# Performance work log

Measured on AMD Instinct MI355X. Metric: run time of the kernel, lower is better.

## Reference

```python
import jax, jax.numpy as jnp
import numpy as np

WS = 8        # window_size
HEADS = 6     # num_heads
DIM = 96      # dim


def _relative_position_index(ws):
    # Static int index table, identical to the torch buffer construction.
    coords = np.stack(np.meshgrid(np.arange(ws), np.arange(ws), indexing='ij'))  # (2, ws, ws)
    cf = coords.reshape(2, -1)                              # (2, N)
    rel = cf[:, :, None] - cf[:, None, :]                   # (2, N, N)
    rel = rel.transpose(1, 2, 0).copy()                     # (N, N, 2)
    rel[:, :, 0] += ws - 1
    rel[:, :, 1] += ws - 1
    rel[:, :, 0] *= 2 * ws - 1
    return rel.sum(-1)                                      # (N, N)


def setup_inputs() -> dict:
    key = jax.random.key(0)
    ks = jax.random.split(key, 6)
    B, C, H, W = 1, DIM, 512, 512
    return {
        'x': jax.random.normal(ks[0], (B, C, H, W), jnp.float32),
        'qkv_w': jax.random.normal(ks[1], (3 * C, C), jnp.float32) * 0.02,
        'qkv_b': jnp.zeros((3 * C,), jnp.float32),
        'dw_w': jax.random.normal(ks[2], (3 * C, 1, 3, 3), jnp.float32) * 0.02,
        'dw_b': jnp.zeros((3 * C,), jnp.float32),
        'proj_w': jax.random.normal(ks[3], (C, C), jnp.float32) * 0.02,
        'proj_b': jnp.zeros((C,), jnp.float32),
        'temperature': jnp.ones((HEADS, 1, 1), jnp.float32),
        'rel_bias_table': jax.random.normal(ks[4], ((2 * WS - 1) ** 2, HEADS), jnp.float32) * 0.02,
    }


def reference(x, qkv_w, qkv_b, dw_w, dw_b, proj_w, proj_b, temperature, rel_bias_table):
    B, C, H, W = x.shape
    ws, heads = WS, HEADS
    N = ws * ws
    hd = C // heads
    scale = hd ** (-0.5)

    # ---- window partition: (B,C,H,W) -> (B*nW, C, ws, ws) ----
    xw = x.reshape(B, C, H // ws, ws, W // ws, ws)
    xw = xw.transpose(0, 2, 4, 1, 3, 5).reshape(-1, C, ws, ws)

    # ---- qkv 1x1 conv + depthwise 3x3 conv ----
    qkv = jnp.einsum('oi,bihw->bohw', qkv_w, xw) + qkv_b[None, :, None, None]
    qkv = jax.lax.conv_general_dilated(
        qkv, dw_w, window_strides=(1, 1), padding='SAME',
        feature_group_count=3 * C,
        dimension_numbers=('NCHW', 'OIHW', 'NCHW')) + dw_b[None, :, None, None]
    q, k, v = jnp.split(qkv, 3, axis=1)

    # (b, head, c, N)
    def to_heads(t):
        return t.reshape(t.shape[0], heads, hd, N)

    q = to_heads(q * scale)
    k = to_heads(k)
    v = to_heads(v)

    # F.normalize(dim=-1): L2 over the spatial (N) axis, eps=1e-12
    q = q / jnp.clip(jnp.linalg.norm(q, axis=-1, keepdims=True), 1e-12)
    k = k / jnp.clip(jnp.linalg.norm(k, axis=-1, keepdims=True), 1e-12)

    # channel attention: (b,h,c,c)
    attn_ch = jnp.einsum('bhcn,bhdn->bhcd', q, k) * temperature
    # spatial attention: (b,h,N,N)
    attn_sp = jnp.einsum('bhcn,bhcm->bhnm', q, k)

    idx = _relative_position_index(ws).reshape(-1)           # (N*N,)
    bias = rel_bias_table[idx].reshape(N, N, heads).transpose(2, 0, 1)  # (h,N,N)
    attn_sp = attn_sp + bias[None]

    attn_ch = jax.nn.softmax(attn_ch, axis=-1)
    attn_sp = jax.nn.softmax(attn_sp, axis=-1)

    # out = attn_channel @ v @ attn : (b,h,c,N)
    out = jnp.einsum('bhcd,bhdn->bhcn', attn_ch, v)
    out = jnp.einsum('bhcn,bhnm->bhcm', out, attn_sp)

    # back to (B*nW, C, ws, ws) then window reverse -> (B,C,H,W)
    out = out.reshape(-1, C, ws, ws)
    out = out.reshape(B, H // ws, W // ws, C, ws, ws)
    out = out.transpose(0, 3, 1, 4, 2, 5).reshape(B, C, H, W)

    # proj 1x1 conv
    out = jnp.einsum('oi,bihw->bohw', proj_w, out) + proj_b[None, :, None, None]
    return out
```

## Files before the change

kernel.cpp:

```cpp
#include <hip/hip_runtime.h>

typedef short short8 __attribute__((ext_vector_type(8)));
typedef float float4v __attribute__((ext_vector_type(4)));

__device__ __forceinline__ unsigned short f2bf(float f) {
    unsigned int u = __float_as_uint(f);
    u += 0x7fffu + ((u >> 16) & 1u);
    return (unsigned short)(u >> 16);
}
__device__ __forceinline__ float bfs(const unsigned short* p) {
    return __uint_as_float(((unsigned int)*p) << 16);
}
__device__ __forceinline__ float4v mfma16(short8 a, short8 b, float4v c) {
    return __builtin_amdgcn_mfma_f32_16x16x32_bf16(a, b, c, 0, 0, 0);
}

__global__ void prep_pack(const float* __restrict__ qkv_w,
                          const float* __restrict__ proj_w,
                          short* __restrict__ apq, short* __restrict__ app) {
    const int i = blockIdx.x * 256 + threadIdx.x;
    if (i < 3456) {
        const int rem = i % 192, f = rem / 64, lane = rem % 64;
        const int m = (i / 192) * 16 + (lane & 15);
        const int kb = f * 32 + ((lane >> 4) & 3) * 8;
        const float* s = qkv_w + m * 96 + kb;
        short8 o;
        #pragma unroll
        for (int j = 0; j < 8; ++j) o[j] = (short)f2bf(s[j]);
        *(short8*)(apq + i * 8) = o;
    } else if (i < 4608) {
        const int i2 = i - 3456;
        const int rem = i2 % 192, f = rem / 64, lane = rem % 64;
        const int m = (i2 / 192) * 16 + (lane & 15);
        const int kb = f * 32 + ((lane >> 4) & 3) * 8;
        const float* s = proj_w + m * 96 + kb;
        short8 o;
        #pragma unroll
        for (int j = 0; j < 8; ++j) o[j] = (short)f2bf(s[j]);
        *(short8*)(app + i2 * 8) = o;
    }
}

__global__ __launch_bounds__(256, 2)
void fused_win_attn(const float* __restrict__ x,
                    const short* __restrict__ apq,
                    const float* __restrict__ qkv_b,
                    const float* __restrict__ dw_w,
                    const float* __restrict__ dw_b,
                    const short* __restrict__ app,
                    const float* __restrict__ proj_b,
                    const float* __restrict__ temperature,
                    const float* __restrict__ rel_bias,
                    float* __restrict__ yout)
{
    __shared__ __align__(16) unsigned char smem[60688];
    unsigned short* sxT   = (unsigned short*)smem;
    unsigned short* soutT = (unsigned short*)(smem + 13312);
    unsigned short* sbias = (unsigned short*)(smem + 26624);
    unsigned short* sqkv  = (unsigned short*)(smem + 29328);
    unsigned short* raw   = (unsigned short*)(smem + 36240);
    unsigned short* sST   = (unsigned short*)(smem + 36240);
    unsigned short* qnT   = (unsigned short*)(smem + 45456);
    unsigned short* knT   = (unsigned short*)(smem + 48528);
    unsigned short* vT    = (unsigned short*)(smem + 51600);
    unsigned short* stmp  = (unsigned short*)(smem + 54672);
    unsigned short* ach   = (unsigned short*)(smem + 56976);
    float*          sdw   = (float*)(smem + 57744);
    float*          sred  = (float*)(smem + 59664);

    const int tid  = threadIdx.x;
    const int lane = tid & 63;
    const int g    = tid >> 6;
    const int quad = lane >> 4;
    const int l15  = lane & 15;
    const int wi   = blockIdx.x;
    const int y0   = (wi >> 6) << 3;
    const int x0   = (wi & 63) << 3;
    const int py   = lane >> 3, px = lane & 7;

    for (int r = tid; r < 1536; r += 256) {
        const int c = r >> 4, q4 = r & 15, p0 = q4 * 4;
        float4 v = *(const float4*)(x + c * 262144 + (y0 + (p0 >> 3)) * 512 + x0 + (p0 & 7));
        sxT[(p0 + 0) * 104 + c] = f2bf(v.x);
        sxT[(p0 + 1) * 104 + c] = f2bf(v.y);
        sxT[(p0 + 2) * 104 + c] = f2bf(v.z);
        sxT[(p0 + 3) * 104 + c] = f2bf(v.w);
    }
    for (int r = tid; r < 1350; r += 256) sbias[r] = f2bf(rel_bias[r]);
    __syncthreads();

    for (int h = 0; h < 6; ++h) {
        for (int r = tid; r < 480; r += 256) {
            const int j = r / 10, t = r % 10;
            const int O = (j >> 4) * 96 + h * 16 + (j & 15);
            sdw[r] = (t < 9) ? dw_w[O * 9 + t] : dw_b[O];
        }
        {
            short8 bf[3];
            #pragma unroll
            for (int f = 0; f < 3; ++f)
                bf[f] = *(const short8*)(sxT + (g * 16 + l15) * 104 + f * 32 + quad * 8);
            #pragma unroll
            for (int t = 0; t < 3; ++t) {
                float4v acc = {0.f, 0.f, 0.f, 0.f};
                #pragma unroll
                for (int f = 0; f < 3; ++f) {
                    short8 af = *(const short8*)(apq + (((t * 6 + h) * 3 + f) * 64 + lane) * 8);
                    acc = mfma16(af, bf[f], acc);
                }
                #pragma unroll
                for (int reg = 0; reg < 4; ++reg) {
                    const int rr = quad * 4 + reg;
                    raw[(t * 16 + rr) * 65 + g * 16 + l15] =
                        f2bf(acc[reg] + qkv_b[t * 96 + h * 16 + rr]);
                }
            }
        }
        __syncthreads();

        #pragma unroll
        for (int r = 0; r < 12; ++r) {
            const int j = g + 4 * r;
            const float v = bfs(raw + j * 65 + lane);
            const float* w = sdw + j * 10;
            float a = w[9];
            #pragma unroll
            for (int di = 0; di < 3; ++di) {
                #pragma unroll
                for (int dj = 0; dj < 3; ++dj) {
                    const int off = (di - 1) * 8 + (dj - 1);
                    const float nb = (off == 0) ? v : __shfl(v, lane + off, 64);
                    const bool ok = ((unsigned)(py + di - 1) < 8u) & ((unsigned)(px + dj - 1) < 8u);
                    a = fmaf(w[di * 3 + dj], ok ? nb : 0.f, a);
                }
            }
            if (j < 32) {
                float ss = a * a;
                #pragma unroll
                for (int m = 1; m < 64; m <<= 1) ss += __shfl_xor(ss, m, 64);
                const float nv = a * (1.f / fmaxf(sqrtf(ss), 1e-12f));
                const unsigned short b = f2bf(nv);
                sqkv[j * 72 + lane] = b;
                if (j < 16) qnT[lane * 24 + j] = b;
                else        knT[lane * 24 + (j - 16)] = b;
            } else {
                vT[lane * 24 + (j - 32)] = f2bf(a);
            }
        }
        __syncthreads();

        float ex[16];
        {
            short8 ak = {0,0,0,0,0,0,0,0};
            if (lane < 32) ak = *(const short8*)(knT + (g * 16 + l15) * 24 + quad * 8);
            #pragma unroll
            for (int nt = 0; nt < 4; ++nt) {
                short8 bq = {0,0,0,0,0,0,0,0};
                if (lane < 32) bq = *(const short8*)(qnT + (nt * 16 + l15) * 24 + quad * 8);
                float4v cs = {0.f, 0.f, 0.f, 0.f};
                cs = mfma16(ak, bq, cs);
                float ps = 0.f;
                #pragma unroll
                for (int reg = 0; reg < 4; ++reg) {
                    const int m = g * 16 + quad * 4 + reg;
                    const int n = nt * 16 + l15;
                    const int idx = ((n >> 3) - (m >> 3) + 7) * 15 + ((n & 7) - (m & 7) + 7);
                    const float e = __expf(cs[reg] + bfs(sbias + idx * 6 + h));
                    ex[nt * 4 + reg] = e;
                    ps += e;
                }
                ps += __shfl_xor(ps, 16, 64);
                ps += __shfl_xor(ps, 32, 64);
                if (lane < 16) sred[g * 64 + nt * 16 + lane] = ps;
            }
        }
        if (g == 0) {
            short8 a0 = *(const short8*)(sqkv + l15 * 72 + quad * 8);
            short8 a1 = *(const short8*)(sqkv + l15 * 72 + 32 + quad * 8);
            short8 b0 = *(const short8*)(sqkv + (16 + l15) * 72 + quad * 8);
            short8 b1 = *(const short8*)(sqkv + (16 + l15) * 72 + 32 + quad * 8);
            float4v cc = {0.f, 0.f, 0.f, 0.f};
            cc = mfma16(a0, b0, cc);
            cc = mfma16(a1, b1, cc);
            const float tp = temperature[h];
            #pragma unroll
            for (int reg = 0; reg < 4; ++reg) {
                const float e = __expf(cc[reg] * tp);
                float se = e;
                #pragma unroll
                for (int m = 1; m < 16; m <<= 1) se += __shfl_xor(se, m, 64);
                ach[(quad * 4 + reg) * 24 + l15] = f2bf(e / se);
            }
        }
        __syncthreads();

        #pragma unroll
        for (int nt = 0; nt < 4; ++nt) {
            const int n = nt * 16 + l15;
            const float inv = 1.f / (sred[n] + sred[64 + n] + sred[128 + n] + sred[192 + n]);
            #pragma unroll
            for (int reg = 0; reg < 4; ++reg)
                sST[(g * 16 + quad * 4 + reg) * 72 + n] = f2bf(ex[nt * 4 + reg] * inv);
        }
        {
            short8 af = {0,0,0,0,0,0,0,0}, bf = {0,0,0,0,0,0,0,0};
            if (lane < 32) {
                af = *(const short8*)(ach + l15 * 24 + quad * 8);
                bf = *(const short8*)(vT + (g * 16 + l15) * 24 + quad * 8);
            }
            float4v ct = {0.f, 0.f, 0.f, 0.f};
            ct = mfma16(af, bf, ct);
            #pragma unroll
            for (int reg = 0; reg < 4; ++reg)
                stmp[(quad * 4 + reg) * 72 + g * 16 + l15] = f2bf(ct[reg]);
        }
        __syncthreads();

        {
            short8 a0 = *(const short8*)(stmp + l15 * 72 + quad * 8);
            short8 a1 = *(const short8*)(stmp + l15 * 72 + 32 + quad * 8);
            short8 b0 = *(const short8*)(sST + (g * 16 + l15) * 72 + quad * 8);
            short8 b1 = *(const short8*)(sST + (g * 16 + l15) * 72 + 32 + quad * 8);
            float4v co = {0.f, 0.f, 0.f, 0.f};
            co = mfma16(a0, b0, co);
            co = mfma16(a1, b1, co);
            #pragma unroll
            for (int reg = 0; reg < 4; ++reg)
                soutT[(g * 16 + l15) * 104 + h * 16 + quad * 4 + reg] = f2bf(co[reg]);
        }
        __syncthreads();
    }

    {
        short8 pb[3];
        #pragma unroll
        for (int f = 0; f < 3; ++f)
            pb[f] = *(const short8*)(soutT + (g * 16 + l15) * 104 + f * 32 + quad * 8);
        const int p = g * 16 + l15;
        float* outbase = yout + (y0 + (p >> 3)) * 512 + x0 + (p & 7);
        #pragma unroll
        for (int mt = 0; mt < 6; ++mt) {
            float4v acc = {0.f, 0.f, 0.f, 0.f};
            #pragma unroll
            for (int f = 0; f < 3; ++f) {
                short8 af = *(const short8*)(app + ((mt * 3 + f) * 64 + lane) * 8);
                acc = mfma16(af, pb[f], acc);
            }
            #pragma unroll
            for (int reg = 0; reg < 4; ++reg) {
                const int o = mt * 16 + quad * 4 + reg;
                outbase[o * 262144] = acc[reg] + proj_b[o];
            }
        }
    }
}

extern "C" void kernel_launch(void* const* d_in, const int* in_sizes, int n_in,
                              void* d_out, int out_size, void* d_ws, size_t ws_size,
                              hipStream_t stream) {
    const float* x      = (const float*)d_in[0];
    const float* qkv_w  = (const float*)d_in[1];
    const float* qkv_b  = (const float*)d_in[2];
    const float* dw_w   = (const float*)d_in[3];
    const float* dw_b   = (const float*)d_in[4];
    const float* proj_w = (const float*)d_in[5];
    const float* proj_b = (const float*)d_in[6];
    const float* temp   = (const float*)d_in[7];
    const float* relb   = (const float*)d_in[8];
    float* o = (float*)d_out;

    short* apq = (short*)d_ws;
    short* app = apq + 27648;

    hipLaunchKernelGGL(prep_pack, dim3(18), dim3(256), 0, stream, qkv_w, proj_w, apq, app);
    hipLaunchKernelGGL(fused_win_attn, dim3(4096), dim3(256), 0, stream,
                       x, apq, qkv_b, dw_w, dw_b, app, proj_b, temp, relb, o);
}
```

Measured before the change: 654.8 us.

## Shrink LDS footprint, pad depthwise conv buffer, and raise occupancy to four blocks

Reorganizes shared memory so buffers alias each other, cutting LDS use from about 60KB to 40KB. This lets launch bounds ask for four resident blocks per CU instead of two. The depthwise 3x3 conv now reads from a zero-padded 10x10 LDS tile with precomputed offsets rather than cross-lane shuffles with boundary masks. Depthwise weights are loaded as wave-uniform scalars from global memory instead of being staged in LDS, and q/k/v are written as packed 4-element stores. Block indices are swizzled to change window traversal order, and the x fragments are hoisted out of the head loop into registers. The tighter register budget at four blocks per CU may cause spills, and the aliased buffers need careful synchronization.

```diff
diff --git a/kernel.cpp b/kernel.cpp
--- a/kernel.cpp
+++ b/kernel.cpp
@@ -41,7 +41,7 @@
     }
 }
 
-__global__ __launch_bounds__(256, 2)
+__global__ __launch_bounds__(256, 4)
 void fused_win_attn(const float* __restrict__ x,
                     const short* __restrict__ apq,
                     const float* __restrict__ qkv_b,
@@ -53,33 +53,33 @@
                     const float* __restrict__ rel_bias,
                     float* __restrict__ yout)
 {
-    __shared__ __align__(16) unsigned char smem[60688];
+    __shared__ __align__(16) unsigned char smem[40080];
     unsigned short* sxT   = (unsigned short*)smem;
+    unsigned short* raw   = (unsigned short*)smem;
+    unsigned short* sST   = (unsigned short*)smem;
+    unsigned short* stmp  = (unsigned short*)(smem + 9216);
+    unsigned short* ach   = (unsigned short*)(smem + 11520);
+    float*          sred  = (float*)(smem + 12288);
     unsigned short* soutT = (unsigned short*)(smem + 13312);
-    unsigned short* sbias = (unsigned short*)(smem + 26624);
-    unsigned short* sqkv  = (unsigned short*)(smem + 29328);
-    unsigned short* raw   = (unsigned short*)(smem + 36240);
-    unsigned short* sST   = (unsigned short*)(smem + 36240);
-    unsigned short* qnT   = (unsigned short*)(smem + 45456);
-    unsigned short* knT   = (unsigned short*)(smem + 48528);
-    unsigned short* vT    = (unsigned short*)(smem + 51600);
-    unsigned short* stmp  = (unsigned short*)(smem + 54672);
-    unsigned short* ach   = (unsigned short*)(smem + 56976);
-    float*          sdw   = (float*)(smem + 57744);
-    float*          sred  = (float*)(smem + 59664);
+    unsigned short* sqkv  = (unsigned short*)(smem + 26624);
+    unsigned short* qnT   = (unsigned short*)(smem + 31232);
+    unsigned short* knT   = (unsigned short*)(smem + 33280);
+    unsigned short* vT    = (unsigned short*)(smem + 35328);
+    unsigned short* sbias = (unsigned short*)(smem + 37376);
 
     const int tid  = threadIdx.x;
     const int lane = tid & 63;
     const int g    = tid >> 6;
     const int quad = lane >> 4;
     const int l15  = lane & 15;
-    const int wi   = blockIdx.x;
-    const int y0   = (wi >> 6) << 3;
-    const int x0   = (wi & 63) << 3;
-    const int py   = lane >> 3, px = lane & 7;
+    const int bx = blockIdx.x;
+    const int wi = (bx & ~15) | ((bx & 7) << 1) | ((bx >> 3) & 1);
+    const int y0 = (wi >> 6) << 3;
+    const int x0 = (wi & 63) << 3;
+    const int py = lane >> 3, px = lane & 7;
 
     for (int r = tid; r < 1536; r += 256) {
-        const int c = r >> 4, q4 = r & 15, p0 = q4 * 4;
+        const int c = r >> 4, p0 = (r & 15) * 4;
         float4 v = *(const float4*)(x + c * 262144 + (y0 + (p0 >> 3)) * 512 + x0 + (p0 & 7));
         sxT[(p0 + 0) * 104 + c] = f2bf(v.x);
         sxT[(p0 + 1) * 104 + c] = f2bf(v.y);
@@ -89,74 +89,93 @@
     for (int r = tid; r < 1350; r += 256) sbias[r] = f2bf(rel_bias[r]);
     __syncthreads();
 
+    short8 bfx[3];
+    #pragma unroll
+    for (int f = 0; f < 3; ++f)
+        bfx[f] = *(const short8*)(sxT + (g * 16 + l15) * 104 + f * 32 + quad * 8);
+    int doff[9];
+    #pragma unroll
+    for (int di = 0; di < 3; ++di)
+        #pragma unroll
+        for (int dj = 0; dj < 3; ++dj)
+            doff[di * 3 + dj] = (py + di) * 10 + (px + dj);
+    __syncthreads();
+
     for (int h = 0; h < 6; ++h) {
-        for (int r = tid; r < 480; r += 256) {
-            const int j = r / 10, t = r % 10;
-            const int O = (j >> 4) * 96 + h * 16 + (j & 15);
-            sdw[r] = (t < 9) ? dw_w[O * 9 + t] : dw_b[O];
-        }
-        {
-            short8 bf[3];
-            #pragma unroll
-            for (int f = 0; f < 3; ++f)
-                bf[f] = *(const short8*)(sxT + (g * 16 + l15) * 104 + f * 32 + quad * 8);
+        for (int r = tid; r < 1728; r += 256) {
+            const int ch = r / 36, k = r % 36;
+            int cell;
+            if (k < 10)      cell = k;
+            else if (k < 20) cell = 90 + (k - 10);
+            else if (k < 28) cell = (k - 19) * 10;
+            else             cell = (k - 27) * 10 + 9;
+            raw[ch * 100 + cell] = 0;
+        }
+        {
+            const int p = g * 16 + l15;
+            const int wcell = (p >> 3) * 10 + (p & 7) + 11;
             #pragma unroll
             for (int t = 0; t < 3; ++t) {
                 float4v acc = {0.f, 0.f, 0.f, 0.f};
                 #pragma unroll
                 for (int f = 0; f < 3; ++f) {
                     short8 af = *(const short8*)(apq + (((t * 6 + h) * 3 + f) * 64 + lane) * 8);
-                    acc = mfma16(af, bf[f], acc);
+                    acc = mfma16(af, bfx[f], acc);
                 }
                 #pragma unroll
                 for (int reg = 0; reg < 4; ++reg) {
                     const int rr = quad * 4 + reg;
-                    raw[(t * 16 + rr) * 65 + g * 16 + l15] =
+                    raw[(t * 16 + rr) * 100 + wcell] =
                         f2bf(acc[reg] + qkv_b[t * 96 + h * 16 + rr]);
                 }
             }
         }
         __syncthreads();
 
-        #pragma unroll
-        for (int r = 0; r < 12; ++r) {
-            const int j = g + 4 * r;
-            const float v = bfs(raw + j * 65 + lane);
-            const float* w = sdw + j * 10;
-            float a = w[9];
-            #pragma unroll
-            for (int di = 0; di < 3; ++di) {
-                #pragma unroll
-                for (int dj = 0; dj < 3; ++dj) {
-                    const int off = (di - 1) * 8 + (dj - 1);
-                    const float nb = (off == 0) ? v : __shfl(v, lane + off, 64);
-                    const bool ok = ((unsigned)(py + di - 1) < 8u) & ((unsigned)(px + dj - 1) < 8u);
-                    a = fmaf(w[di * 3 + dj], ok ? nb : 0.f, a);
-                }
-            }
-            if (j < 32) {
-                float ss = a * a;
-                #pragma unroll
-                for (int m = 1; m < 64; m <<= 1) ss += __shfl_xor(ss, m, 64);
-                const float nv = a * (1.f / fmaxf(sqrtf(ss), 1e-12f));
-                const unsigned short b = f2bf(nv);
-                sqkv[j * 72 + lane] = b;
-                if (j < 16) qnT[lane * 24 + j] = b;
-                else        knT[lane * 24 + (j - 16)] = b;
-            } else {
-                vT[lane * 24 + (j - 32)] = f2bf(a);
-            }
+        {
+            unsigned int qw0 = 0, qw1 = 0, kw0 = 0, kw1 = 0, vw0 = 0, vw1 = 0;
+            #pragma unroll
+            for (int r = 0; r < 12; ++r) {
+                const int j = (r >> 2) * 16 + 4 * g + (r & 3);
+                const int O = __builtin_amdgcn_readfirstlane((j >> 4) * 96 + h * 16 + (j & 15));
+                const float* wq = dw_w + O * 9;
+                float a = dw_b[O];
+                const unsigned short* rbase = raw + j * 100;
+                #pragma unroll
+                for (int t = 0; t < 9; ++t)
+                    a = fmaf(wq[t], bfs(rbase + doff[t]), a);
+                if (r < 8) {
+                    float ss = a * a;
+                    #pragma unroll
+                    for (int m = 1; m < 64; m <<= 1) ss += __shfl_xor(ss, m, 64);
+                    a = a * (1.f / fmaxf(sqrtf(ss), 1e-12f));
+                    sqkv[j * 72 + lane] = f2bf(a);
+                }
+                const unsigned int bv = f2bf(a);
+                if      (r == 0)  qw0 |= bv;          else if (r == 1)  qw0 |= bv << 16;
+                else if (r == 2)  qw1 |= bv;          else if (r == 3)  qw1 |= bv << 16;
+                else if (r == 4)  kw0 |= bv;          else if (r == 5)  kw0 |= bv << 16;
+                else if (r == 6)  kw1 |= bv;          else if (r == 7)  kw1 |= bv << 16;
+                else if (r == 8)  vw0 |= bv;          else if (r == 9)  vw0 |= bv << 16;
+                else if (r == 10) vw1 |= bv;          else              vw1 |= bv << 16;
+            }
+            uint2 uq; uq.x = qw0; uq.y = qw1;
+            uint2 uk; uk.x = kw0; uk.y = kw1;
+            uint2 uv; uv.x = vw0; uv.y = vw1;
+            *(uint2*)(qnT + lane * 16 + 4 * g) = uq;
+            *(uint2*)(knT + lane * 16 + 4 * g) = uk;
+            *(uint2*)(vT  + lane * 16 + 4 * g) = uv;
         }
         __syncthreads();
 
         float ex[16];
         {
-            short8 ak = {0,0,0,0,0,0,0,0};
-            if (lane < 32) ak = *(const short8*)(knT + (g * 16 + l15) * 24 + quad * 8);
+            short8 ak = {0, 0, 0, 0, 0, 0, 0, 0};
+            if (lane < 32) ak = *(const short8*)(knT + (g * 16 + l15) * 16 + quad * 8);
             #pragma unroll
             for (int nt = 0; nt < 4; ++nt) {
-                short8 bq = {0,0,0,0,0,0,0,0};
-                if (lane < 32) bq = *(const short8*)(qnT + (nt * 16 + l15) * 24 + quad * 8);
+                short8 bq = {0, 0, 0, 0, 0, 0, 0, 0};
+                if (lane < 32) bq = *(const short8*)(qnT + (nt * 16 + l15) * 16 + quad * 8);
                 float4v cs = {0.f, 0.f, 0.f, 0.f};
                 cs = mfma16(ak, bq, cs);
                 float ps = 0.f;
@@ -203,13 +222,13 @@
                 sST[(g * 16 + quad * 4 + reg) * 72 + n] = f2bf(ex[nt * 4 + reg] * inv);
         }
         {
-            short8 af = {0,0,0,0,0,0,0,0}, bf = {0,0,0,0,0,0,0,0};
+            short8 af = {0, 0, 0, 0, 0, 0, 0, 0}, bv = {0, 0, 0, 0, 0, 0, 0, 0};
             if (lane < 32) {
                 af = *(const short8*)(ach + l15 * 24 + quad * 8);
-                bf = *(const short8*)(vT + (g * 16 + l15) * 24 + quad * 8);
+                bv = *(const short8*)(vT + (g * 16 + l15) * 16 + quad * 8);
             }
             float4v ct = {0.f, 0.f, 0.f, 0.f};
-            ct = mfma16(af, bf, ct);
+            ct = mfma16(af, bv, ct);
             #pragma unroll
             for (int reg = 0; reg < 4; ++reg)
                 stmp[(quad * 4 + reg) * 72 + g * 16 + l15] = f2bf(ct[reg]);
```

Measured after the change: 689.4 us. 5.3% more time.
